# Kernel optimization log

Hardware: AMD Instinct MI355X
Metric: run time of the kernel (lower is better)

The kernel has to match this reference:

```python
import jax, jax.numpy as jnp
import numpy as np

B, SQ, SK, DK, DV = 8, 2048, 2048, 256, 256
EPS = 1e-7  # keras.backend.epsilon()


def setup_inputs() -> dict:
    key = jax.random.key(0)
    kq, kk, kv, km = jax.random.split(key, 4)
    query = jax.random.normal(kq, (B, SQ, DK), dtype=jnp.float32)
    k_ = jax.random.normal(kk, (B, SK, DK), dtype=jnp.float32)
    value = jax.random.normal(kv, (B, SK, DV), dtype=jnp.float32)
    mask = jax.random.uniform(km, (B, SK)) > 0.1
    return {"query": query, "key": k_, "value": value, "mask": mask}


def reference(query, key, value, mask):
    d = query.shape[-1]
    # scores: [B, Sq, Sk]
    e = jnp.einsum('bqd,bkd->bqk', query, key) / jnp.sqrt(jnp.asarray(d, query.dtype))
    # original applies exp(e - max) BEFORE masking (non-standard but faithful)
    e = jnp.exp(e - jnp.max(e, axis=-1, keepdims=True))
    q_len, k_len = query.shape[1], key.shape[1]
    causal = (jnp.arange(k_len)[None, :] <= jnp.arange(q_len)[:, None]).astype(query.dtype)
    e = e * causal[None, :, :]                       # history_only mask
    e = e * mask[:, None, :].astype(query.dtype)     # key padding mask
    a = e / (jnp.sum(e, axis=-1, keepdims=True) + EPS)
    return jnp.einsum('bqk,bkv->bqv', a, value)
```

## Files before the change

kernel.cpp:

```cpp
#include <hip/hip_runtime.h>
#include <hip/hip_bf16.h>

#define B_   8
#define SQ_  2048
#define SK_  2048
#define DK_  256
#define DV_  256

#define KT    32
#define PSTR  40
#define TELEM (KT * DK_)

typedef __bf16 bf16x8 __attribute__((ext_vector_type(8)));
typedef float  f32x4  __attribute__((ext_vector_type(4)));

__device__ __forceinline__ void gl_lds16(const void* g, void* l) {
    __builtin_amdgcn_global_load_lds(
        (const __attribute__((address_space(1))) void*)g,
        (__attribute__((address_space(3))) void*)l, 16, 0, 0);
}

__global__ __launch_bounds__(256)
void make_ktiles(const float* __restrict__ K, __bf16* __restrict__ Kt)
{
    const int t = blockIdx.x, b = blockIdx.y;
    __bf16* out = Kt + ((size_t)(b * 64 + t)) * TELEM;
    const float* src = K + ((size_t)(b * SK_ + t * KT)) * DK_;
    #pragma unroll
    for (int it = 0; it < 4; ++it) {
        int ci  = it * 256 + threadIdx.x;
        int dk8 = ci >> 5;
        int key = ci & 31;
        const float* p = src + (size_t)key * DK_ + dk8 * 8;
        float4 f0 = *(const float4*)(p);
        float4 f1 = *(const float4*)(p + 4);
        bf16x8 o;
        o[0] = (__bf16)f0.x; o[1] = (__bf16)f0.y; o[2] = (__bf16)f0.z; o[3] = (__bf16)f0.w;
        o[4] = (__bf16)f1.x; o[5] = (__bf16)f1.y; o[6] = (__bf16)f1.z; o[7] = (__bf16)f1.w;
        *(bf16x8*)(out + (size_t)ci * 8) = o;
    }
}

__global__ __launch_bounds__(256)
void make_vtiles(const float* __restrict__ V, __bf16* __restrict__ Vt)
{
    const int t = blockIdx.x, b = blockIdx.y;
    __bf16* out = Vt + ((size_t)(b * 64 + t)) * TELEM;
    const float* src = V + ((size_t)(b * SK_ + t * KT)) * DV_;
    #pragma unroll
    for (int it = 0; it < 4; ++it) {
        int ci  = it * 256 + threadIdx.x;
        int kc8 = ci >> 8;
        int dv  = ci & 255;
        const float* p = src + (size_t)(kc8 * 8) * DV_ + dv;
        bf16x8 o;
        #pragma unroll
        for (int j = 0; j < 8; ++j)
            o[j] = (__bf16)p[(size_t)j * DV_];
        *(bf16x8*)(out + (size_t)ci * 8) = o;
    }
}

__global__ __launch_bounds__(256, 4)
void attn_fwd(const float* __restrict__ Qg, const __bf16* __restrict__ Kt,
              const __bf16* __restrict__ Vt, const void* __restrict__ Mv,
              __bf16* __restrict__ Opart, float* __restrict__ Lpart,
              int tpc, int slotcap, int nch)
{
    __shared__ __align__(16) __bf16 sK[TELEM];
    __shared__ __align__(16) __bf16 sV[TELEM];
    __shared__ __align__(16) __bf16 sP[4][16 * PSTR];

    const int tid  = threadIdx.x;
    const int wv   = tid >> 6;
    const int lane = tid & 63;
    const int quad = lane >> 4;
    const int l16  = lane & 15;

    const int b = blockIdx.x;
    const int y = (nch - 1) - blockIdx.y;

    int g = 0;
    while ((tpc >> 2) * (g + 1) * (g + 2) <= y) ++g;
    const int rem = y - (tpc >> 2) * g * (g + 1);
    const int jq  = rem / (g + 1);
    const int qb  = g * (tpc >> 1) + jq;
    const int s   = rem - jq * (g + 1);
    const int nt  = 2 * qb + 2;
    const int nc  = g + 1;
    const int t0  = nt * s / nc;
    const int t1  = nt * (s + 1) / nc;

    const int qrow = qb * 64 + wv * 16;

    const unsigned char* Mb = (const unsigned char*)Mv;
    const int*           Mi = (const int*)Mv;
    int nzb = 0;
    {
        const unsigned int* mw = (const unsigned int*)Mv;
        #pragma unroll
        for (int i = 0; i < 32; ++i) {
            unsigned int w = mw[i];
            nzb += ((w & 0x000000ffu) != 0) + ((w & 0x0000ff00u) != 0)
                 + ((w & 0x00ff0000u) != 0) + ((w & 0xff000000u) != 0);
        }
    }
    const bool mask_byte = (nzb > 40);

    bf16x8 qfrag[8];
    {
        const float* qp = Qg + ((size_t)(b * SQ_ + qrow + l16)) * DK_ + quad * 8;
        #pragma unroll
        for (int kt = 0; kt < 8; ++kt) {
            float4 f0 = *(const float4*)(qp + kt * 32);
            float4 f1 = *(const float4*)(qp + kt * 32 + 4);
            bf16x8 q;
            q[0] = (__bf16)f0.x; q[1] = (__bf16)f0.y; q[2] = (__bf16)f0.z; q[3] = (__bf16)f0.w;
            q[4] = (__bf16)f1.x; q[5] = (__bf16)f1.y; q[6] = (__bf16)f1.z; q[7] = (__bf16)f1.w;
            qfrag[kt] = q;
        }
    }

    f32x4 oacc[16];
    #pragma unroll
    for (int v = 0; v < 16; ++v) oacc[v] = (f32x4){0.f, 0.f, 0.f, 0.f};
    float lsum[4] = {0.f, 0.f, 0.f, 0.f};

    const __bf16* Kbase = Kt + (size_t)b * 64 * TELEM;
    const __bf16* Vbase = Vt + (size_t)b * 64 * TELEM;
    const size_t  mbase = (size_t)b * SK_;

    for (int t = t0; t < t1; ++t) {
        __syncthreads();

        const __bf16* kt_g = Kbase + (size_t)t * TELEM;
        const __bf16* vt_g = Vbase + (size_t)t * TELEM;
        #pragma unroll
        for (int r = 0; r < 4; ++r) {
            int ci = r * 256 + tid;
            gl_lds16(kt_g + (size_t)ci * 8, (char*)sK + ci * 16);
        }
        #pragma unroll
        for (int r = 0; r < 4; ++r) {
            int ci = r * 256 + tid;
            gl_lds16(vt_g + (size_t)ci * 8, (char*)sV + ci * 16);
        }
        __syncthreads();

        const int k0 = t * KT;

        f32x4 s0 = {0.f,0.f,0.f,0.f}, s1 = {0.f,0.f,0.f,0.f};
        #pragma unroll
        for (int kt = 0; kt < 8; ++kt) {
            bf16x8 b0 = *(const bf16x8*)&sK[(size_t)((kt * 4 + quad) * 32 + l16)      * 8];
            bf16x8 b1 = *(const bf16x8*)&sK[(size_t)((kt * 4 + quad) * 32 + 16 + l16) * 8];
            s0 = __builtin_amdgcn_mfma_f32_16x16x32_bf16(qfrag[kt], b0, s0, 0, 0, 0);
            s1 = __builtin_amdgcn_mfma_f32_16x16x32_bf16(qfrag[kt], b1, s1, 0, 0, 0);
        }

        #pragma unroll
        for (int nf = 0; nf < 2; ++nf) {
            f32x4 sv = (nf == 0) ? s0 : s1;
            int key = k0 + nf * 16 + l16;
            float mk = mask_byte ? (Mb[mbase + key] ? 1.0f : 0.0f)
                                 : (Mi[mbase + key] ? 1.0f : 0.0f);
            #pragma unroll
            for (int i = 0; i < 4; ++i) {
                int qr = qrow + quad * 4 + i;
                float p = __expf(sv[i] * 0.0625f);
                p = (key <= qr) ? (p * mk) : 0.0f;
                lsum[i] += p;
                sP[wv][(quad * 4 + i) * PSTR + nf * 16 + l16] = (__bf16)p;
            }
        }
        asm volatile("s_waitcnt lgkmcnt(0)" ::: "memory");
        __builtin_amdgcn_wave_barrier();

        {
            bf16x8 pa = *(const bf16x8*)&sP[wv][l16 * PSTR + quad * 8];
            #pragma unroll
            for (int vf = 0; vf < 16; ++vf) {
                bf16x8 bv = *(const bf16x8*)&sV[(size_t)(quad * 256 + vf * 16 + l16) * 8];
                oacc[vf] = __builtin_amdgcn_mfma_f32_16x16x32_bf16(pa, bv, oacc[vf], 0, 0, 0);
            }
        }
    }

    const size_t slot = ((size_t)(b * 32 + qb)) * slotcap + s;
    #pragma unroll
    for (int i = 0; i < 4; ++i) {
        float v = lsum[i];
        v += __shfl_xor(v, 1);
        v += __shfl_xor(v, 2);
        v += __shfl_xor(v, 4);
        v += __shfl_xor(v, 8);
        lsum[i] = v;
    }
    if (l16 == 0) {
        #pragma unroll
        for (int i = 0; i < 4; ++i)
            Lpart[slot * 64 + wv * 16 + quad * 4 + i] = lsum[i];
    }
    __bf16* ob = Opart + slot * (64 * 256);
    #pragma unroll
    for (int vf = 0; vf < 16; ++vf) {
        #pragma unroll
        for (int i = 0; i < 4; ++i)
            ob[(wv * 16 + quad * 4 + i) * 256 + vf * 16 + l16] = (__bf16)oacc[vf][i];
    }
}

__global__ __launch_bounds__(512)
void attn_reduce(const __bf16* __restrict__ Opart, const float* __restrict__ Lpart,
                 float* __restrict__ Og, int tpc, int slotcap)
{
    const int b  = blockIdx.x;
    const int qb = blockIdx.y;
    const int chunks = (2 * qb + 2 + tpc - 1) / tpc;
    const int tid = threadIdx.x;
    const int row = tid >> 3;
    const int cg  = tid & 7;

    const size_t sbase = ((size_t)(b * 32 + qb)) * slotcap;
    float acc[32];
    #pragma unroll
    for (int i = 0; i < 32; ++i) acc[i] = 0.f;
    float ls = 0.f;

    for (int s = 0; s < chunks; ++s) {
        const __bf16* p = Opart + (sbase + s) * (64 * 256) + row * 256 + cg * 32;
        #pragma unroll
        for (int v = 0; v < 4; ++v) {
            bf16x8 x = *(const bf16x8*)(p + v * 8);
            #pragma unroll
            for (int e = 0; e < 8; ++e) acc[v * 8 + e] += (float)x[e];
        }
        ls += Lpart[(sbase + s) * 64 + row];
    }
    const float inv = 1.0f / (ls + 1e-7f);
    float* op = Og + ((size_t)b * SQ_ + qb * 64 + row) * DV_ + cg * 32;
    #pragma unroll
    for (int v = 0; v < 8; ++v) {
        float4 o;
        o.x = acc[v * 4 + 0] * inv; o.y = acc[v * 4 + 1] * inv;
        o.z = acc[v * 4 + 2] * inv; o.w = acc[v * 4 + 3] * inv;
        *(float4*)(op + v * 4) = o;
    }
}

extern "C" void kernel_launch(void* const* d_in, const int* in_sizes, int n_in,
                              void* d_out, int out_size, void* d_ws, size_t ws_size,
                              hipStream_t stream) {
    const float* Q = (const float*)d_in[0];
    const float* K = (const float*)d_in[1];
    const float* V = (const float*)d_in[2];
    const void*  M = d_in[3];
    float* Out = (float*)d_out;

    __bf16* Ktl = (__bf16*)d_ws;
    __bf16* Vtl = Ktl + (size_t)B_ * 64 * TELEM;
    __bf16* Opart = Vtl + (size_t)B_ * 64 * TELEM;

    auto need = [](int slotcap) -> size_t {
        return (size_t)(16 * 1024 * 1024)
             + (size_t)256 * slotcap * 64 * 256 * 2
             + (size_t)256 * slotcap * 64 * 4;
    };
    int tpc, slotcap, nch;
    if      (ws_size >= need(8)) { tpc = 8;  slotcap = 8; nch = 144; }
    else if (ws_size >= need(4)) { tpc = 16; slotcap = 4; nch = 80;  }
    else                         { tpc = 64; slotcap = 1; nch = 32;  }

    float* Lpart = (float*)(Opart + (size_t)256 * slotcap * 64 * 256);

    make_ktiles<<<dim3(64, B_), dim3(256), 0, stream>>>(K, Ktl);
    make_vtiles<<<dim3(64, B_), dim3(256), 0, stream>>>(V, Vtl);

    attn_fwd<<<dim3(B_, nch), dim3(256), 0, stream>>>(Q, Ktl, Vtl, M, Opart, Lpart,
                                                      tpc, slotcap, nch);
    attn_reduce<<<dim3(B_, 32), dim3(512), 0, stream>>>(Opart, Lpart, Out, tpc, slotcap);
}
```

Before: 156.6 us.

## Double-buffer K/V tiles, grow blocks to 128 query rows, fuse tile prep

The attention kernel now uses 512-thread blocks covering 128 query rows, so each K/V tile in LDS is shared by twice as many waves. K/V tile loads are double-buffered, with the next tile prefetched during compute and one barrier per iteration instead of two. The K and V bf16 conversion kernels are merged into a single launch, and the reduce kernel is split into half-column blocks with rewritten chunk/slot mapping. This doubles LDS use per block and lowers the number of blocks, which can reduce occupancy and load balance for the causal work split.

```diff
diff --git a/kernel.cpp b/kernel.cpp
--- a/kernel.cpp
+++ b/kernel.cpp
@@ -10,6 +10,7 @@
 #define KT    32
 #define PSTR  40
 #define TELEM (KT * DK_)
+#define NQB   16
 
 typedef __bf16 bf16x8 __attribute__((ext_vector_type(8)));
 typedef float  f32x4  __attribute__((ext_vector_type(4)));
@@ -21,55 +22,54 @@
 }
 
 __global__ __launch_bounds__(256)
-void make_ktiles(const float* __restrict__ K, __bf16* __restrict__ Kt)
+void make_tiles(const float* __restrict__ K, const float* __restrict__ V,
+                __bf16* __restrict__ Kt, __bf16* __restrict__ Vt)
 {
     const int t = blockIdx.x, b = blockIdx.y;
-    __bf16* out = Kt + ((size_t)(b * 64 + t)) * TELEM;
-    const float* src = K + ((size_t)(b * SK_ + t * KT)) * DK_;
-    #pragma unroll
-    for (int it = 0; it < 4; ++it) {
-        int ci  = it * 256 + threadIdx.x;
-        int dk8 = ci >> 5;
-        int key = ci & 31;
-        const float* p = src + (size_t)key * DK_ + dk8 * 8;
-        float4 f0 = *(const float4*)(p);
-        float4 f1 = *(const float4*)(p + 4);
-        bf16x8 o;
-        o[0] = (__bf16)f0.x; o[1] = (__bf16)f0.y; o[2] = (__bf16)f0.z; o[3] = (__bf16)f0.w;
-        o[4] = (__bf16)f1.x; o[5] = (__bf16)f1.y; o[6] = (__bf16)f1.z; o[7] = (__bf16)f1.w;
-        *(bf16x8*)(out + (size_t)ci * 8) = o;
-    }
-}
-
-__global__ __launch_bounds__(256)
-void make_vtiles(const float* __restrict__ V, __bf16* __restrict__ Vt)
-{
-    const int t = blockIdx.x, b = blockIdx.y;
-    __bf16* out = Vt + ((size_t)(b * 64 + t)) * TELEM;
-    const float* src = V + ((size_t)(b * SK_ + t * KT)) * DV_;
-    #pragma unroll
-    for (int it = 0; it < 4; ++it) {
-        int ci  = it * 256 + threadIdx.x;
-        int kc8 = ci >> 8;
-        int dv  = ci & 255;
-        const float* p = src + (size_t)(kc8 * 8) * DV_ + dv;
-        bf16x8 o;
-        #pragma unroll
-        for (int j = 0; j < 8; ++j)
-            o[j] = (__bf16)p[(size_t)j * DV_];
-        *(bf16x8*)(out + (size_t)ci * 8) = o;
-    }
-}
-
-__global__ __launch_bounds__(256, 4)
+    {
+        __bf16* out = Kt + ((size_t)(b * 64 + t)) * TELEM;
+        const float* src = K + ((size_t)(b * SK_ + t * KT)) * DK_;
+        #pragma unroll
+        for (int it = 0; it < 4; ++it) {
+            int ci  = it * 256 + threadIdx.x;
+            int dk8 = ci >> 5;
+            int key = ci & 31;
+            const float* p = src + (size_t)key * DK_ + dk8 * 8;
+            float4 f0 = *(const float4*)(p);
+            float4 f1 = *(const float4*)(p + 4);
+            bf16x8 o;
+            o[0] = (__bf16)f0.x; o[1] = (__bf16)f0.y; o[2] = (__bf16)f0.z; o[3] = (__bf16)f0.w;
+            o[4] = (__bf16)f1.x; o[5] = (__bf16)f1.y; o[6] = (__bf16)f1.z; o[7] = (__bf16)f1.w;
+            *(bf16x8*)(out + (size_t)ci * 8) = o;
+        }
+    }
+    {
+        __bf16* out = Vt + ((size_t)(b * 64 + t)) * TELEM;
+        const float* src = V + ((size_t)(b * SK_ + t * KT)) * DV_;
+        #pragma unroll
+        for (int it = 0; it < 4; ++it) {
+            int ci  = it * 256 + threadIdx.x;
+            int kc8 = ci >> 8;
+            int dv  = ci & 255;
+            const float* p = src + (size_t)(kc8 * 8) * DV_ + dv;
+            bf16x8 o;
+            #pragma unroll
+            for (int j = 0; j < 8; ++j)
+                o[j] = (__bf16)p[(size_t)j * DV_];
+            *(bf16x8*)(out + (size_t)ci * 8) = o;
+        }
+    }
+}
+
+__global__ __launch_bounds__(512, 4)
 void attn_fwd(const float* __restrict__ Qg, const __bf16* __restrict__ Kt,
               const __bf16* __restrict__ Vt, const void* __restrict__ Mv,
               __bf16* __restrict__ Opart, float* __restrict__ Lpart,
-              int tpc, int slotcap, int nch)
+              int tpc, int slotcap)
 {
-    __shared__ __align__(16) __bf16 sK[TELEM];
-    __shared__ __align__(16) __bf16 sV[TELEM];
-    __shared__ __align__(16) __bf16 sP[4][16 * PSTR];
+    __shared__ __align__(16) __bf16 sK[2][TELEM];
+    __shared__ __align__(16) __bf16 sV[2][TELEM];
+    __shared__ __align__(16) __bf16 sP[8][16 * PSTR];
 
     const int tid  = threadIdx.x;
     const int wv   = tid >> 6;
@@ -78,20 +78,19 @@
     const int l16  = lane & 15;
 
     const int b = blockIdx.x;
-    const int y = (nch - 1) - blockIdx.y;
-
-    int g = 0;
-    while ((tpc >> 2) * (g + 1) * (g + 2) <= y) ++g;
-    const int rem = y - (tpc >> 2) * g * (g + 1);
-    const int jq  = rem / (g + 1);
-    const int qb  = g * (tpc >> 1) + jq;
-    const int s   = rem - jq * (g + 1);
-    const int nt  = 2 * qb + 2;
-    const int nc  = g + 1;
-    const int t0  = nt * s / nc;
-    const int t1  = nt * (s + 1) / nc;
-
-    const int qrow = qb * 64 + wv * 16;
+
+    int yy = blockIdx.y, qb = 0, s = 0;
+    for (int q = NQB - 1; q >= 0; --q) {
+        int c = (4 * (q + 1) + tpc - 1) / tpc;
+        if (yy < c) { qb = q; s = yy; break; }
+        yy -= c;
+    }
+    const int nt = 4 * (qb + 1);
+    const int nc = (nt + tpc - 1) / tpc;
+    const int t0 = nt * s / nc;
+    const int t1 = nt * (s + 1) / nc;
+
+    const int qrow = qb * 128 + wv * 16;
 
     const unsigned char* Mb = (const unsigned char*)Mv;
     const int*           Mi = (const int*)Mv;
@@ -130,30 +129,38 @@
     const __bf16* Vbase = Vt + (size_t)b * 64 * TELEM;
     const size_t  mbase = (size_t)b * SK_;
 
+    {
+        const __bf16* kg = Kbase + (size_t)t0 * TELEM;
+        const __bf16* vg = Vbase + (size_t)t0 * TELEM;
+        #pragma unroll
+        for (int r = 0; r < 2; ++r) {
+            int ci = r * 512 + tid;
+            gl_lds16(kg + (size_t)ci * 8, (char*)&sK[0][0] + ci * 16);
+            gl_lds16(vg + (size_t)ci * 8, (char*)&sV[0][0] + ci * 16);
+        }
+    }
+    __syncthreads();
+
+    int cur = 0;
     for (int t = t0; t < t1; ++t) {
-        __syncthreads();
-
-        const __bf16* kt_g = Kbase + (size_t)t * TELEM;
-        const __bf16* vt_g = Vbase + (size_t)t * TELEM;
-        #pragma unroll
-        for (int r = 0; r < 4; ++r) {
-            int ci = r * 256 + tid;
-            gl_lds16(kt_g + (size_t)ci * 8, (char*)sK + ci * 16);
-        }
-        #pragma unroll
-        for (int r = 0; r < 4; ++r) {
-            int ci = r * 256 + tid;
-            gl_lds16(vt_g + (size_t)ci * 8, (char*)sV + ci * 16);
-        }
-        __syncthreads();
+        if (t + 1 < t1) {
+            const __bf16* kg = Kbase + (size_t)(t + 1) * TELEM;
+            const __bf16* vg = Vbase + (size_t)(t + 1) * TELEM;
+            #pragma unroll
+            for (int r = 0; r < 2; ++r) {
+                int ci = r * 512 + tid;
+                gl_lds16(kg + (size_t)ci * 8, (char*)&sK[cur ^ 1][0] + ci * 16);
+                gl_lds16(vg + (size_t)ci * 8, (char*)&sV[cur ^ 1][0] + ci * 16);
+            }
+        }
 
         const int k0 = t * KT;
 
         f32x4 s0 = {0.f,0.f,0.f,0.f}, s1 = {0.f,0.f,0.f,0.f};
         #pragma unroll
         for (int kt = 0; kt < 8; ++kt) {
-            bf16x8 b0 = *(const bf16x8*)&sK[(size_t)((kt * 4 + quad) * 32 + l16)      * 8];
-            bf16x8 b1 = *(const bf16x8*)&sK[(size_t)((kt * 4 + quad) * 32 + 16 + l16) * 8];
+            bf16x8 b0 = *(const bf16x8*)&sK[cur][(size_t)((kt * 4 + quad) * 32 + l16)      * 8];
+            bf16x8 b1 = *(const bf16x8*)&sK[cur][(size_t)((kt * 4 + quad) * 32 + 16 + l16) * 8];
             s0 = __builtin_amdgcn_mfma_f32_16x16x32_bf16(qfrag[kt], b0, s0, 0, 0, 0);
             s1 = __builtin_amdgcn_mfma_f32_16x16x32_bf16(qfrag[kt], b1, s1, 0, 0, 0);
         }
@@ -180,13 +187,16 @@
             bf16x8 pa = *(const bf16x8*)&sP[wv][l16 * PSTR + quad * 8];
             #pragma unroll
             for (int vf = 0; vf < 16; ++vf) {
-                bf16x8 bv = *(const bf16x8*)&sV[(size_t)(quad * 256 + vf * 16 + l16) * 8];
+                bf16x8 bv = *(const bf16x8*)&sV[cur][(size_t)(quad * 256 + vf * 16 + l16) * 8];
                 oacc[vf] = __builtin_amdgcn_mfma_f32_16x16x32_bf16(pa, bv, oacc[vf], 0, 0, 0);
             }
         }
-    }
-
-    const size_t slot = ((size_t)(b * 32 + qb)) * slotcap + s;
+
+        __syncthreads();
+        cur ^= 1;
+    }
+
+    const size_t slot = ((size_t)(b * NQB + qb)) * slotcap + s;
     #pragma unroll
     for (int i = 0; i < 4; ++i) {
         float v = lsum[i];
@@ -199,9 +209,9 @@
     if (l16 == 0) {
         #pragma unroll
         for (int i = 0; i < 4; ++i)
-            Lpart[slot * 64 + wv * 16 + quad * 4 + i] = lsum[i];
-    }
-    __bf16* ob = Opart + slot * (64 * 256);
+            Lpart[slot * 128 + wv * 16 + quad * 4 + i] = lsum[i];
+    }
+    __bf16* ob = Opart + slot * (size_t)(128 * 256);
     #pragma unroll
     for (int vf = 0; vf < 16; ++vf) {
         #pragma unroll
@@ -214,33 +224,37 @@
 void attn_reduce(const __bf16* __restrict__ Opart, const float* __restrict__ Lpart,
                  float* __restrict__ Og, int tpc, int slotcap)
 {
-    const int b  = blockIdx.x;
-    const int qb = blockIdx.y;
-    const int chunks = (2 * qb + 2 + tpc - 1) / tpc;
-    const int tid = threadIdx.x;
-    const int row = tid >> 3;
-    const int cg  = tid & 7;
-
-    const size_t sbase = ((size_t)(b * 32 + qb)) * slotcap;
-    float acc[32];
-    #pragma unroll
-    for (int i = 0; i < 32; ++i) acc[i] = 0.f;
+    const int b    = blockIdx.x;
+    const int y    = blockIdx.y;
+    const int qb64 = y >> 1;
+    const int half = y & 1;
+    const int qb   = qb64 >> 1;
+    const int rowbase = (qb64 & 1) * 64;
+    const int nt   = 4 * (qb + 1);
+    const int chunks = (nt + tpc - 1) / tpc;
+    const int tid  = threadIdx.x;
+    const int row  = tid >> 3;
+    const int cg   = tid & 7;
+
+    const size_t sbase = ((size_t)(b * NQB + qb)) * slotcap;
+    float acc[16];
+    #pragma unroll
+    for (int i = 0; i < 16; ++i) acc[i] = 0.f;
     float ls = 0.f;
 
     for (int s = 0; s < chunks; ++s) {
-        const __bf16* p = Opart + (sbase + s) * (64 * 256) + row * 256 + cg * 32;
-        #pragma unroll
-        for (int v = 0; v < 4; ++v) {
-            bf16x8 x = *(const bf16x8*)(p + v * 8);
-            #pragma unroll
-            for (int e = 0; e < 8; ++e) acc[v * 8 + e] += (float)x[e];
-        }
-        ls += Lpart[(sbase + s) * 64 + row];
+        const __bf16* p = Opart + (sbase + s) * (size_t)(128 * 256)
+                        + (size_t)(rowbase + row) * 256 + half * 128 + cg * 16;
+        bf16x8 x0 = *(const bf16x8*)(p);
+        bf16x8 x1 = *(const bf16x8*)(p + 8);
+        #pragma unroll
+        for (int e = 0; e < 8; ++e) { acc[e] += (float)x0[e]; acc[8 + e] += (float)x1[e]; }
+        ls += Lpart[(sbase + s) * 128 + rowbase + row];
     }
     const float inv = 1.0f / (ls + 1e-7f);
-    float* op = Og + ((size_t)b * SQ_ + qb * 64 + row) * DV_ + cg * 32;
-    #pragma unroll
-    for (int v = 0; v < 8; ++v) {
+    float* op = Og + ((size_t)b * SQ_ + qb64 * 64 + row) * DV_ + half * 128 + cg * 16;
+    #pragma unroll
+    for (int v = 0; v < 4; ++v) {
         float4 o;
         o.x = acc[v * 4 + 0] * inv; o.y = acc[v * 4 + 1] * inv;
         o.z = acc[v * 4 + 2] * inv; o.w = acc[v * 4 + 3] * inv;
@@ -263,20 +277,20 @@
 
     auto need = [](int slotcap) -> size_t {
         return (size_t)(16 * 1024 * 1024)
-             + (size_t)256 * slotcap * 64 * 256 * 2
-             + (size_t)256 * slotcap * 64 * 4;
+             + (size_t)(B_ * NQB) * slotcap * (128 * 256) * 2
+             + (size_t)(B_ * NQB) * slotcap * 128 * 4;
     };
-    int tpc, slotcap, nch;
-    if      (ws_size >= need(8)) { tpc = 8;  slotcap = 8; nch = 144; }
-    else if (ws_size >= need(4)) { tpc = 16; slotcap = 4; nch = 80;  }
-    else                         { tpc = 64; slotcap = 1; nch = 32;  }
-
-    float* Lpart = (float*)(Opart + (size_t)256 * slotcap * 64 * 256);
-
-    make_ktiles<<<dim3(64, B_), dim3(256), 0, stream>>>(K, Ktl);
-    make_vtiles<<<dim3(64, B_), dim3(256), 0, stream>>>(V, Vtl);
-
-    attn_fwd<<<dim3(B_, nch), dim3(256), 0, stream>>>(Q, Ktl, Vtl, M, Opart, Lpart,
-                                                      tpc, slotcap, nch);
-    attn_reduce<<<dim3(B_, 32), dim3(512), 0, stream>>>(Opart, Lpart, Out, tpc, slotcap);
-}
+    int tpc, slotcap;
+    if      (ws_size >= need(8)) { tpc = 8;  slotcap = 8; }
+    else if (ws_size >= need(4)) { tpc = 16; slotcap = 4; }
+    else                         { tpc = 64; slotcap = 1; }
+    int nch = 0;
+    for (int q = 0; q < NQB; ++q) nch += (4 * (q + 1) + tpc - 1) / tpc;
+
+    float* Lpart = (float*)(Opart + (size_t)(B_ * NQB) * slotcap * (128 * 256));
+
+    make_tiles<<<dim3(64, B_), dim3(256), 0, stream>>>(K, V, Ktl, Vtl);
+    attn_fwd<<<dim3(B_, nch), dim3(512), 0, stream>>>(Q, Ktl, Vtl, M, Opart, Lpart,
+                                                      tpc, slotcap);
+    attn_reduce<<<dim3(B_, 64), dim3(512), 0, stream>>>(Opart, Lpart, Out, tpc, slotcap);
+}
```

After: 152.5 us. 2.6% less time.
